# Performance work log

Measured on AMD Instinct MI355X. Metric: run time of the kernel, lower is better.

Reference implementation:

```python
import jax, jax.numpy as jnp
import numpy as np

B, N, H = 128, 1024, 128          # graphs, nodes per graph, hidden size
K1, K2, K3 = 512, 256, 128        # ceil(ratio^l * N), ratio = 0.5
DEG = 8                           # avg degree
E = B * N * DEG                   # total edges (fixed, masked after pooling)


def gcn_conv(x, row, col, mask, W, b, n):
    h = x @ W
    deg = jax.ops.segment_sum(mask, col, num_segments=n) + 1.0  # + self loop
    dinv = jax.lax.rsqrt(deg)
    coef = (dinv[row] * dinv[col] * mask)[:, None]
    agg = jax.ops.segment_sum(h[row] * coef, col, num_segments=n)
    return agg + h * (dinv * dinv)[:, None] + b  # self-loop term + bias


def topk_pool(x, row, col, mask, p, n_graphs, n_per, k):
    # PyG TopKPooling: y = x.p/||p||, keep per-graph top-k, x' = x[perm]*tanh(y[perm])
    score = (x @ p) / jnp.linalg.norm(p)
    vals, idx = jax.lax.top_k(score.reshape(n_graphs, n_per), k)  # [B, k]
    sel = (idx + (jnp.arange(n_graphs) * n_per)[:, None]).reshape(-1)
    xs = x[sel] * jnp.tanh(vals.reshape(-1))[:, None]
    # relabel edges; drop edges touching removed nodes via mask
    newid = jnp.full((n_graphs * n_per,), -1, jnp.int32).at[sel].set(
        jnp.arange(n_graphs * k, dtype=jnp.int32))
    nr, nc = newid[row], newid[col]
    nmask = mask * ((nr >= 0) & (nc >= 0)).astype(mask.dtype)
    return xs, jnp.maximum(nr, 0), jnp.maximum(nc, 0), nmask


def readout(x, n_graphs, k):
    # cat([gmp, gap]) with contiguous equal-size graphs
    xg = x.reshape(n_graphs, k, -1)
    return jnp.concatenate([xg.max(axis=1), xg.mean(axis=1)], axis=1)


def _forward(x, edge_row, edge_col, W1, b1, p1, W2, b2, p2, W3, b3, p3):
    mask = jnp.ones((E,), x.dtype)
    h = jax.nn.relu(gcn_conv(x, edge_row, edge_col, mask, W1, b1, B * N))
    x1, r, c, m = topk_pool(h, edge_row, edge_col, mask, p1, B, N, K1)
    out = readout(x1, B, K1)
    h = jax.nn.relu(gcn_conv(x1, r, c, m, W2, b2, B * K1))
    x2, r, c, m = topk_pool(h, r, c, m, p2, B, K1, K2)
    out = out + readout(x2, B, K2)
    h = jax.nn.relu(gcn_conv(x2, r, c, m, W3, b3, B * K2))
    x3, r, c, m = topk_pool(h, r, c, m, p3, B, K2, K3)
    out = out + readout(x3, B, K3)
    return out  # [B, 2*H]


def setup_inputs() -> dict:
    key = jax.random.key(0)
    ks = jax.random.split(key, 12)
    x = jax.random.normal(ks[0], (B * N, H), jnp.float32)
    off = (jnp.arange(B, dtype=jnp.int32) * N)[:, None]
    edge_row = (jax.random.randint(ks[1], (B, N * DEG), 0, N, jnp.int32) + off).reshape(-1)
    edge_col = (jax.random.randint(ks[2], (B, N * DEG), 0, N, jnp.int32) + off).reshape(-1)
    s = 1.0 / np.sqrt(H)
    params = {}
    for i, tag in enumerate(["1", "2", "3"]):
        params["W" + tag] = jax.random.normal(ks[3 + 3 * i], (H, H), jnp.float32) * s
        params["b" + tag] = jnp.zeros((H,), jnp.float32)
        params["p" + tag] = jax.random.normal(ks[4 + 3 * i], (H,), jnp.float32)
    return {"x": x, "edge_row": edge_row, "edge_col": edge_col, **params}


def reference(x, edge_row, edge_col, W1, b1, p1, W2, b2, p2, W3, b3, p3):
    return _forward(x, edge_row, edge_col, W1, b1, p1, W2, b2, p2, W3, b3, p3)
```

## Files before the change

kernel.cpp:

```cpp
#include <hip/hip_runtime.h>
#include <math.h>

#define BG   128
#define NPER 1024
#define HDIM 128
#define NEDGE (BG * NPER * 8)
#define NMAX (BG * NPER)
#define EPG  (NEDGE / BG)
#define CAP  48
#define PRE  16
#define CROWS 64

typedef __attribute__((ext_vector_type(8))) short s16x8;
typedef __attribute__((ext_vector_type(4))) float f32x4;

static __device__ __forceinline__ ushort f2bf(float f) {
  uint u = __float_as_uint(f);
  return (ushort)((u + 0x7fffu + ((u >> 16) & 1u)) >> 16);
}
static __device__ __forceinline__ float bf2f(ushort h) {
  return __uint_as_float(((uint)h) << 16);
}


__global__ __launch_bounds__(256) void countfill_kernel(
    const int* __restrict__ cr, const int* __restrict__ cc,
    int* __restrict__ cnt, int* __restrict__ meta8,
    int* __restrict__ srcext, int mask) {
  int e = blockIdx.x * 256 + threadIdx.x;
  int c = cc[e];
  int rl = cr[e] & mask;
  int pos = atomicAdd(&cnt[c], 1);
  if (pos < PRE) {
    meta8[(size_t)c * PRE + pos] = rl;
  } else if (pos < CAP) {
    srcext[(size_t)c * CAP + pos] = rl;
  }
}

extern __shared__ float ldsbuf[];


__global__ __launch_bounds__(1024) void agg_lds_kernel(
    const float* __restrict__ x, float* __restrict__ z,
    const int* __restrict__ meta8, const int* __restrict__ srcext,
    const int* __restrict__ deg, int npg) {
  float* sX = ldsbuf;
  float* sDinv = sX + npg * 32;
  int g = blockIdx.x >> 2;
  int chunk = blockIdx.x & 3;
  int t = threadIdx.x;
  int base = g * npg;

  const float4* x4 = (const float4*)x;
  float4* sX4 = (float4*)sX;
  for (int i = t; i < npg * 8; i += 1024) {
    int r = i >> 3, l8 = i & 7;
    float dv = rsqrtf((float)deg[base + r] + 1.0f);
    float4 v = x4[(size_t)(base + r) * 32 + chunk * 8 + l8];
    v.x *= dv; v.y *= dv; v.z *= dv; v.w *= dv;
    sX4[i] = v;
  }
  for (int i = t; i < npg; i += 1024)
    sDinv[i] = rsqrtf((float)deg[base + i] + 1.0f);
  __syncthreads();

  int dl = t >> 3, l = t & 7;
  int base8 = (t & 63) & 56;
  const int2* m2 = (const int2*)meta8;
  for (int dst = dl; dst < npg; dst += 128) {
    int node = base + dst;
    int2 mq = m2[(size_t)node * 8 + l];
    int d = deg[node];
    if (d > CAP) d = CAP;
    float dc = sDinv[dst];
    float4 a0 = sX4[dst * 8 + l];
    float4 a1 = make_float4(0.f, 0.f, 0.f, 0.f);
    int dp = d < PRE ? d : PRE;
    int e = 0;
    for (; e + 1 < dp; e += 2) {
      int sl = base8 + (e >> 1);
      int si0 = __shfl(mq.x, sl);
      int si1 = __shfl(mq.y, sl);
      float4 v0 = sX4[si0 * 8 + l];
      float4 v1 = sX4[si1 * 8 + l];
      a0.x += v0.x; a0.y += v0.y; a0.z += v0.z; a0.w += v0.w;
      a1.x += v1.x; a1.y += v1.y; a1.z += v1.z; a1.w += v1.w;
    }
    if (e < dp) {
      int sl = base8 + (e >> 1);
      int si0 = __shfl(mq.x, sl);
      float4 v0 = sX4[si0 * 8 + l];
      a0.x += v0.x; a0.y += v0.y; a0.z += v0.z; a0.w += v0.w;
    }
    for (int e2 = PRE; e2 < d; ++e2) {
      int rl = srcext[(size_t)node * CAP + e2];
      float4 v0 = sX4[rl * 8 + l];
      a0.x += v0.x; a0.y += v0.y; a0.z += v0.z; a0.w += v0.w;
    }
    float4 o = make_float4((a0.x + a1.x) * dc, (a0.y + a1.y) * dc,
                           (a0.z + a1.z) * dc, (a0.w + a1.w) * dc);
    ((float4*)z)[(size_t)node * 32 + chunk * 8 + l] = o;
  }
}


__global__ __launch_bounds__(256) void wsplit_kernel(
    const float* __restrict__ W0, const float* __restrict__ W1,
    const float* __restrict__ W2, ushort* __restrict__ wpk) {
  int id = blockIdx.x * 256 + threadIdx.x;
  int L = id >> 14;
  int r = id & 16383;
  int i = r & 7;
  int lane = (r >> 3) & 63;
  int nt = (r >> 9) & 7;
  int kt = (r >> 12) & 3;
  int k = kt * 32 + (lane >> 4) * 8 + i;
  int n = nt * 16 + (lane & 15);
  const float* W = (L == 0) ? W0 : (L == 1) ? W1 : W2;
  float v = W[k * HDIM + n];
  ushort h = f2bf(v);
  float r1 = v - bf2f(h);
  ushort m = f2bf(r1);
  ushort lo = f2bf(r1 - bf2f(m));
  size_t base = (size_t)L * 3 * 16384 + (size_t)r;
  wpk[base] = h;
  wpk[base + 16384] = m;
  wpk[base + 32768] = lo;
}


__global__ __launch_bounds__(256) void conv_mfma_kernel(
    float* __restrict__ zh, const ushort* __restrict__ wpk,
    const float* __restrict__ bias, const float* __restrict__ p,
    float* __restrict__ score) {
  int t = threadIdx.x;
  int wv = t >> 6, l = t & 63;
  int lr = l & 15, lq = l >> 4;
  int arow = blockIdx.x * CROWS + wv * 16 + lr;
  const float* zrow = zh + (size_t)arow * HDIM + lq * 8;

  s16x8 ah[4], am[4], al[4];
  #pragma unroll
  for (int kt = 0; kt < 4; ++kt) {
    float4 v0 = ((const float4*)(zrow + kt * 32))[0];
    float4 v1 = ((const float4*)(zrow + kt * 32))[1];
    float f[8] = {v0.x, v0.y, v0.z, v0.w, v1.x, v1.y, v1.z, v1.w};
    #pragma unroll
    for (int i = 0; i < 8; ++i) {
      ushort h = f2bf(f[i]);
      float r1 = f[i] - bf2f(h);
      ushort m = f2bf(r1);
      ushort lo = f2bf(r1 - bf2f(m));
      ah[kt][i] = (short)h; am[kt][i] = (short)m; al[kt][i] = (short)lo;
    }
  }

  f32x4 acc[8];
  #pragma unroll
  for (int nt = 0; nt < 8; ++nt) acc[nt] = (f32x4)(0.f);

  const s16x8* wh = (const s16x8*)wpk;
  const s16x8* wm = wh + 2048;
  const s16x8* wl = wm + 2048;

  #pragma unroll
  for (int kt = 0; kt < 4; ++kt) {
    #pragma unroll
    for (int nt = 0; nt < 8; ++nt) {
      int fi = (kt * 8 + nt) * 64 + l;
      s16x8 bh = wh[fi];
      s16x8 bm = wm[fi];
      s16x8 bl = wl[fi];
      acc[nt] = __builtin_amdgcn_mfma_f32_16x16x32_bf16(ah[kt], bh, acc[nt], 0, 0, 0);
      acc[nt] = __builtin_amdgcn_mfma_f32_16x16x32_bf16(ah[kt], bm, acc[nt], 0, 0, 0);
      acc[nt] = __builtin_amdgcn_mfma_f32_16x16x32_bf16(am[kt], bh, acc[nt], 0, 0, 0);
      acc[nt] = __builtin_amdgcn_mfma_f32_16x16x32_bf16(ah[kt], bl, acc[nt], 0, 0, 0);
      acc[nt] = __builtin_amdgcn_mfma_f32_16x16x32_bf16(al[kt], bh, acc[nt], 0, 0, 0);
      acc[nt] = __builtin_amdgcn_mfma_f32_16x16x32_bf16(am[kt], bm, acc[nt], 0, 0, 0);
    }
  }

  int orow = blockIdx.x * CROWS + wv * 16 + lq * 4;
  float part[4] = {0.f, 0.f, 0.f, 0.f};
  #pragma unroll
  for (int nt = 0; nt < 8; ++nt) {
    float bv = bias[nt * 16 + lr];
    float pv = p[nt * 16 + lr];
    #pragma unroll
    for (int j = 0; j < 4; ++j) {
      float hv = fmaxf(acc[nt][j] + bv, 0.f);
      part[j] += hv * pv;
      zh[(size_t)(orow + j) * HDIM + nt * 16 + lr] = hv;
    }
  }
  #pragma unroll
  for (int j = 0; j < 4; ++j) {
    #pragma unroll
    for (int s = 1; s < 16; s <<= 1) part[j] += __shfl_xor(part[j], s);
    if (lr == 0) score[orow + j] = part[j];
  }
}


__global__ __launch_bounds__(1024) void topk_mega_kernel(
    const float* __restrict__ score, const float* __restrict__ p,
    const float* __restrict__ h, float* __restrict__ xo,
    const int* __restrict__ in_r, const int* __restrict__ in_c,
    int* __restrict__ out_r, int* __restrict__ out_c,
    int* __restrict__ meta8, int* __restrict__ srcext,
    int* __restrict__ cnt, float* __restrict__ acc,
    float* __restrict__ outf, int P, int K, int L) {
  __shared__ float sv[1024];
  __shared__ int si[1024];
  __shared__ int snew[1024];
  __shared__ int scnt[512];
  __shared__ float s_pn;
  __shared__ float4 smx[32][32], ssm[32][32];
  int g = blockIdx.x;
  int t = threadIdx.x;

  if (L < 2 && t < 512) scnt[t] = 0;
  snew[t] = -1;
  if (t < 128) { float v = p[t]; sv[t] = v * v; }
  __syncthreads();
  for (int off = 64; off; off >>= 1) {
    if (t < off) sv[t] += sv[t + off];
    __syncthreads();
  }
  if (t == 0) s_pn = sqrtf(sv[0]);
  __syncthreads();
  float pn = s_pn;

  sv[t] = score[(size_t)g * P + t];
  si[t] = t;
  for (int size = 2; size <= P; size <<= 1) {
    for (int stride = size >> 1; stride; stride >>= 1) {
      __syncthreads();
      int j = t ^ stride;
      if (j > t) {
        float a = sv[t], b = sv[j];
        int ia = si[t], ib = si[j];
        bool tFirst = (a > b) || (a == b && ia < ib);
        bool up = ((t & size) == 0);
        if (up ? !tFirst : tFirst) {
          sv[t] = b; sv[j] = a;
          si[t] = ib; si[j] = ia;
        }
      }
    }
  }
  __syncthreads();
  if (t < K) {
    snew[si[t]] = t;
    sv[t] = tanhf(sv[t] / pn);
  }
  __syncthreads();

  int lane = t & 31, grp = t >> 5;
  const float4* h4 = (const float4*)h;
  float4* xo4 = (float4*)xo;
  size_t hbase = (size_t)g * P * 32;
  float4 mx = make_float4(-INFINITY, -INFINITY, -INFINITY, -INFINITY);
  float4 sm = make_float4(0.f, 0.f, 0.f, 0.f);
  #pragma unroll
  for (int i = 0; i < 16; ++i) {
    int j = grp * 16 + i;
    float th = sv[j];
    float4 v = h4[hbase + (size_t)si[j] * 32 + lane];
    v.x *= th; v.y *= th; v.z *= th; v.w *= th;
    xo4[((size_t)g * K + j) * 32 + lane] = v;
    mx.x = fmaxf(mx.x, v.x); mx.y = fmaxf(mx.y, v.y);
    mx.z = fmaxf(mx.z, v.z); mx.w = fmaxf(mx.w, v.w);
    sm.x += v.x; sm.y += v.y; sm.z += v.z; sm.w += v.w;
  }
  smx[grp][lane] = mx;
  ssm[grp][lane] = sm;
  __syncthreads();
  int ngrp = P >> 5;
  if (grp == 0) {
    for (int s2 = 1; s2 < ngrp; ++s2) {
      float4 m2 = smx[s2][lane], s3 = ssm[s2][lane];
      mx.x = fmaxf(mx.x, m2.x); mx.y = fmaxf(mx.y, m2.y);
      mx.z = fmaxf(mx.z, m2.z); mx.w = fmaxf(mx.w, m2.w);
      sm.x += s3.x; sm.y += s3.y; sm.z += s3.z; sm.w += s3.w;
    }
    int c0 = lane * 4;
    if (L < 2) {
      float* amax = acc + (size_t)L * BG * 256 + (size_t)g * 256;
      float* asum = amax + 128;
      amax[c0 + 0] = mx.x; amax[c0 + 1] = mx.y;
      amax[c0 + 2] = mx.z; amax[c0 + 3] = mx.w;
      asum[c0 + 0] = sm.x; asum[c0 + 1] = sm.y;
      asum[c0 + 2] = sm.z; asum[c0 + 3] = sm.w;
    } else {
      sv[c0 + 0] = mx.x; sv[c0 + 1] = mx.y;
      sv[c0 + 2] = mx.z; sv[c0 + 3] = mx.w;
      sv[128 + c0 + 0] = sm.x; sv[128 + c0 + 1] = sm.y;
      sv[128 + c0 + 2] = sm.z; sv[128 + c0 + 3] = sm.w;
    }
  }

  if (L == 2) {
    __syncthreads();
    float v;
    const float* a0 = acc + (size_t)g * 256;
    const float* a1 = acc + (size_t)BG * 256 + (size_t)g * 256;
    if (t < 128) {
      v = a0[t] + a1[t] + sv[t];
    } else {
      v = a0[t] * (1.f / 512.f) + a1[t] * (1.f / 256.f) + sv[t] * (1.f / 128.f);
    }
    outf[g * 256 + t] = v;
    return;
  }

  int ept = EPG / P;
  int ebase = g * EPG;
  for (int i = 0; i < ept; ++i) {
    int e = ebase + i * P + t;
    int r = in_r[e];
    int nr = -1, nc = -1;
    if (r >= 0) {
      nr = snew[r & (P - 1)];
      nc = snew[in_c[e] & (P - 1)];
    }
    bool ok = (nr >= 0) && (nc >= 0);
    out_r[e] = ok ? g * K + nr : -1;
    out_c[e] = ok ? g * K + nc : -1;
    if (ok) {
      int pos = atomicAdd(&scnt[nc], 1);
      size_t gnode = (size_t)g * K + nc;
      if (pos < PRE) {
        meta8[gnode * PRE + pos] = nr;
      } else if (pos < CAP) {
        srcext[gnode * CAP + pos] = nr;
      }
    }
  }
  __syncthreads();
  if (t < K) cnt[g * K + t] = scnt[t];
}


extern "C" void kernel_launch(void* const* d_in, const int* in_sizes, int n_in,
                              void* d_out, int out_size, void* d_ws, size_t ws_size,
                              hipStream_t stream) {
  const float* x0 = (const float*)d_in[0];
  const int* erow = (const int*)d_in[1];
  const int* ecol = (const int*)d_in[2];
  const float* Wm[3] = {(const float*)d_in[3], (const float*)d_in[6], (const float*)d_in[9]};
  const float* bm[3] = {(const float*)d_in[4], (const float*)d_in[7], (const float*)d_in[10]};
  const float* pm[3] = {(const float*)d_in[5], (const float*)d_in[8], (const float*)d_in[11]};

  char* w = (char*)d_ws;
  size_t off = 0;
  auto alloc = [&](size_t bytes) -> void* {
    void* ptr = w + off;
    off = (off + bytes + 255) & ~(size_t)255;
    return ptr;
  };
  int* cur_row = (int*)alloc((size_t)NEDGE * 4);
  int* cur_col = (int*)alloc((size_t)NEDGE * 4);
  int* meta8   = (int*)alloc((size_t)NMAX * PRE * 4);
  int* srcext  = (int*)alloc((size_t)NMAX * CAP * 4);
  int* cnt     = (int*)alloc((size_t)NMAX * 4);
  float* score = (float*)alloc((size_t)NMAX * 4);
  float* acc   = (float*)alloc((size_t)2 * BG * 256 * 4);
  float* zh    = (float*)alloc((size_t)NMAX * HDIM * 4);
  float* x1    = (float*)alloc((size_t)BG * 512 * HDIM * 4);
  float* x2    = (float*)alloc((size_t)BG * 256 * HDIM * 4);
  float* x3    = (float*)alloc((size_t)BG * 128 * HDIM * 4);
  ushort* wpk  = (ushort*)alloc((size_t)3 * 3 * 16384 * 2);

  hipFuncSetAttribute((const void*)agg_lds_kernel,
                      hipFuncAttributeMaxDynamicSharedMemorySize, 152 * 1024);

  hipMemsetAsync(cnt, 0, (size_t)NMAX * 4, stream);
  countfill_kernel<<<NEDGE / 256, 256, 0, stream>>>(erow, ecol, cnt, meta8,
                                                    srcext, NPER - 1);
  wsplit_kernel<<<(3 * 16384) / 256, 256, 0, stream>>>(Wm[0], Wm[1], Wm[2], wpk);

  const float* xin = x0;
  float* xout[3] = {x1, x2, x3};
  int Ps[3] = {1024, 512, 256};

  for (int L = 0; L < 3; ++L) {
    int P = Ps[L];
    int K = P >> 1;
    int n = BG * P;
    const int* in_r = (L == 0) ? erow : cur_row;
    const int* in_c = (L == 0) ? ecol : cur_col;
    size_t ldsBytes = (size_t)(P * 33) * 4;

    agg_lds_kernel<<<BG * 4, 1024, ldsBytes, stream>>>(
        xin, zh, meta8, srcext, cnt, P);
    conv_mfma_kernel<<<n / CROWS, 256, 0, stream>>>(
        zh, wpk + (size_t)L * 3 * 16384, bm[L], pm[L], score);
    topk_mega_kernel<<<BG, P, 0, stream>>>(
        score, pm[L], zh, xout[L], in_r, in_c, cur_row, cur_col,
        meta8, srcext, cnt, acc, (float*)d_out, P, K, L);
    xin = xout[L];
  }
}
```

Before: 373.7 us.

## Split LDS aggregation into eight feature chunks per graph with 4-wide edge unroll

The LDS-staged GCN aggregation now splits each graph's 128 features into eight 16-float chunks instead of four 32-float chunks. That halves LDS use per block (about 68KB at P=1024 instead of about 135KB) and doubles the block count, so more blocks can be resident per CU. Each destination node now uses 4 lanes instead of 8. Neighbour indices are read as int4 and unrolled four at a time with four accumulators, giving more LDS loads in flight. The cost is that the graph's degree and metadata are read twice as often in total, and lanes sit idle when a node has fewer neighbours.

```diff
diff --git a/kernel.cpp b/kernel.cpp
--- a/kernel.cpp
+++ b/kernel.cpp
@@ -46,18 +46,18 @@
     const int* __restrict__ meta8, const int* __restrict__ srcext,
     const int* __restrict__ deg, int npg) {
   float* sX = ldsbuf;
-  float* sDinv = sX + npg * 32;
-  int g = blockIdx.x >> 2;
-  int chunk = blockIdx.x & 3;
+  float* sDinv = sX + npg * 16;
+  int g = blockIdx.x >> 3;
+  int chunk = blockIdx.x & 7;
   int t = threadIdx.x;
   int base = g * npg;
 
   const float4* x4 = (const float4*)x;
   float4* sX4 = (float4*)sX;
-  for (int i = t; i < npg * 8; i += 1024) {
-    int r = i >> 3, l8 = i & 7;
+  for (int i = t; i < npg * 4; i += 1024) {
+    int r = i >> 2, j = i & 3;
     float dv = rsqrtf((float)deg[base + r] + 1.0f);
-    float4 v = x4[(size_t)(base + r) * 32 + chunk * 8 + l8];
+    float4 v = x4[(size_t)(base + r) * 32 + chunk * 4 + j];
     v.x *= dv; v.y *= dv; v.z *= dv; v.w *= dv;
     sX4[i] = v;
   }
@@ -65,42 +65,63 @@
     sDinv[i] = rsqrtf((float)deg[base + i] + 1.0f);
   __syncthreads();
 
-  int dl = t >> 3, l = t & 7;
-  int base8 = (t & 63) & 56;
-  const int2* m2 = (const int2*)meta8;
-  for (int dst = dl; dst < npg; dst += 128) {
+  int dl = t >> 2, l = t & 3;
+  int base4 = (t & 63) & 60;
+  const int4* m4 = (const int4*)meta8;
+  for (int dst = dl; dst < npg; dst += 256) {
     int node = base + dst;
-    int2 mq = m2[(size_t)node * 8 + l];
+    int4 mq = m4[(size_t)node * 4 + l];
     int d = deg[node];
     if (d > CAP) d = CAP;
     float dc = sDinv[dst];
-    float4 a0 = sX4[dst * 8 + l];
+    float4 a0 = sX4[dst * 4 + l];
     float4 a1 = make_float4(0.f, 0.f, 0.f, 0.f);
+    float4 a2 = make_float4(0.f, 0.f, 0.f, 0.f);
+    float4 a3 = make_float4(0.f, 0.f, 0.f, 0.f);
     int dp = d < PRE ? d : PRE;
-    int e = 0;
-    for (; e + 1 < dp; e += 2) {
-      int sl = base8 + (e >> 1);
-      int si0 = __shfl(mq.x, sl);
-      int si1 = __shfl(mq.y, sl);
-      float4 v0 = sX4[si0 * 8 + l];
-      float4 v1 = sX4[si1 * 8 + l];
+    int full = dp & ~3;
+    for (int e4 = 0; e4 < full; e4 += 4) {
+      int sl = base4 + (e4 >> 2);
+      int s0 = __shfl(mq.x, sl);
+      int s1 = __shfl(mq.y, sl);
+      int s2 = __shfl(mq.z, sl);
+      int s3 = __shfl(mq.w, sl);
+      float4 v0 = sX4[s0 * 4 + l];
+      float4 v1 = sX4[s1 * 4 + l];
+      float4 v2 = sX4[s2 * 4 + l];
+      float4 v3 = sX4[s3 * 4 + l];
       a0.x += v0.x; a0.y += v0.y; a0.z += v0.z; a0.w += v0.w;
       a1.x += v1.x; a1.y += v1.y; a1.z += v1.z; a1.w += v1.w;
-    }
-    if (e < dp) {
-      int sl = base8 + (e >> 1);
-      int si0 = __shfl(mq.x, sl);
-      float4 v0 = sX4[si0 * 8 + l];
+      a2.x += v2.x; a2.y += v2.y; a2.z += v2.z; a2.w += v2.w;
+      a3.x += v3.x; a3.y += v3.y; a3.z += v3.z; a3.w += v3.w;
+    }
+    int rem = dp - full;
+    if (rem) {
+      int sl = base4 + (full >> 2);
+      int s0 = __shfl(mq.x, sl);
+      int s1 = __shfl(mq.y, sl);
+      int s2 = __shfl(mq.z, sl);
+      float4 v0 = sX4[s0 * 4 + l];
       a0.x += v0.x; a0.y += v0.y; a0.z += v0.z; a0.w += v0.w;
+      if (rem > 1) {
+        float4 v1 = sX4[s1 * 4 + l];
+        a1.x += v1.x; a1.y += v1.y; a1.z += v1.z; a1.w += v1.w;
+      }
+      if (rem > 2) {
+        float4 v2 = sX4[s2 * 4 + l];
+        a2.x += v2.x; a2.y += v2.y; a2.z += v2.z; a2.w += v2.w;
+      }
     }
     for (int e2 = PRE; e2 < d; ++e2) {
       int rl = srcext[(size_t)node * CAP + e2];
-      float4 v0 = sX4[rl * 8 + l];
+      float4 v0 = sX4[rl * 4 + l];
       a0.x += v0.x; a0.y += v0.y; a0.z += v0.z; a0.w += v0.w;
     }
-    float4 o = make_float4((a0.x + a1.x) * dc, (a0.y + a1.y) * dc,
-                           (a0.z + a1.z) * dc, (a0.w + a1.w) * dc);
-    ((float4*)z)[(size_t)node * 32 + chunk * 8 + l] = o;
+    float4 o = make_float4((a0.x + a1.x + a2.x + a3.x) * dc,
+                           (a0.y + a1.y + a2.y + a3.y) * dc,
+                           (a0.z + a1.z + a2.z + a3.z) * dc,
+                           (a0.w + a1.w + a2.w + a3.w) * dc);
+    ((float4*)z)[(size_t)node * 32 + chunk * 4 + l] = o;
   }
 }
 
@@ -374,7 +395,7 @@
   ushort* wpk  = (ushort*)alloc((size_t)3 * 3 * 16384 * 2);
 
   hipFuncSetAttribute((const void*)agg_lds_kernel,
-                      hipFuncAttributeMaxDynamicSharedMemorySize, 152 * 1024);
+                      hipFuncAttributeMaxDynamicSharedMemorySize, 72 * 1024);
 
   hipMemsetAsync(cnt, 0, (size_t)NMAX * 4, stream);
   countfill_kernel<<<NEDGE / 256, 256, 0, stream>>>(erow, ecol, cnt, meta8,
@@ -391,9 +412,9 @@
     int n = BG * P;
     const int* in_r = (L == 0) ? erow : cur_row;
     const int* in_c = (L == 0) ? ecol : cur_col;
-    size_t ldsBytes = (size_t)(P * 33) * 4;
-
-    agg_lds_kernel<<<BG * 4, 1024, ldsBytes, stream>>>(
+    size_t ldsBytes = (size_t)(P * 17) * 4;
+
+    agg_lds_kernel<<<BG * 8, 1024, ldsBytes, stream>>>(
         xin, zh, meta8, srcext, cnt, P);
     conv_mfma_kernel<<<n / CROWS, 256, 0, stream>>>(
         zh, wpk + (size_t)L * 3 * 16384, bm[L], pm[L], score);
```

New measurement: 393.3 us. 5.2% more time.

## Remap agg blocks by XCD and unroll two-node branchless neighbor gather

Applied to the files above, without the earlier changes.

Each XCD now handles a contiguous set of graphs through a remapped block index, which is meant to improve L2 locality. The aggregation loop processes two destination nodes per thread group. Each thread loads all 16 prefetched neighbor indices with int4 loads instead of shuffles, and accumulates with mask-multiplied FMAs over a fully unrolled PRE loop. This adds ILP and removes shuffle and loop-branch overhead, at the cost of always doing 16 LDS reads per node, more registers, and an assumption that npg is a multiple of 256 and a power of two.

```diff
diff --git a/kernel.cpp b/kernel.cpp
--- a/kernel.cpp
+++ b/kernel.cpp
@@ -47,10 +47,13 @@
     const int* __restrict__ deg, int npg) {
   float* sX = ldsbuf;
   float* sDinv = sX + npg * 32;
-  int g = blockIdx.x >> 2;
-  int chunk = blockIdx.x & 3;
+  int b = blockIdx.x;
+  int xcd = b & 7, li = b >> 3;
+  int g = xcd * 16 + (li >> 2);
+  int chunk = li & 3;
   int t = threadIdx.x;
   int base = g * npg;
+  int nmask = npg - 1;
 
   const float4* x4 = (const float4*)x;
   float4* sX4 = (float4*)sX;
@@ -66,41 +69,78 @@
   __syncthreads();
 
   int dl = t >> 3, l = t & 7;
-  int base8 = (t & 63) & 56;
-  const int2* m2 = (const int2*)meta8;
-  for (int dst = dl; dst < npg; dst += 128) {
-    int node = base + dst;
-    int2 mq = m2[(size_t)node * 8 + l];
-    int d = deg[node];
-    if (d > CAP) d = CAP;
-    float dc = sDinv[dst];
-    float4 a0 = sX4[dst * 8 + l];
-    float4 a1 = make_float4(0.f, 0.f, 0.f, 0.f);
-    int dp = d < PRE ? d : PRE;
-    int e = 0;
-    for (; e + 1 < dp; e += 2) {
-      int sl = base8 + (e >> 1);
-      int si0 = __shfl(mq.x, sl);
-      int si1 = __shfl(mq.y, sl);
-      float4 v0 = sX4[si0 * 8 + l];
-      float4 v1 = sX4[si1 * 8 + l];
-      a0.x += v0.x; a0.y += v0.y; a0.z += v0.z; a0.w += v0.w;
-      a1.x += v1.x; a1.y += v1.y; a1.z += v1.z; a1.w += v1.w;
-    }
-    if (e < dp) {
-      int sl = base8 + (e >> 1);
-      int si0 = __shfl(mq.x, sl);
-      float4 v0 = sX4[si0 * 8 + l];
-      a0.x += v0.x; a0.y += v0.y; a0.z += v0.z; a0.w += v0.w;
-    }
-    for (int e2 = PRE; e2 < d; ++e2) {
-      int rl = srcext[(size_t)node * CAP + e2];
-      float4 v0 = sX4[rl * 8 + l];
-      a0.x += v0.x; a0.y += v0.y; a0.z += v0.z; a0.w += v0.w;
-    }
-    float4 o = make_float4((a0.x + a1.x) * dc, (a0.y + a1.y) * dc,
-                           (a0.z + a1.z) * dc, (a0.w + a1.w) * dc);
-    ((float4*)z)[(size_t)node * 32 + chunk * 8 + l] = o;
+  const int4* m4 = (const int4*)meta8;
+  float4* z4 = (float4*)z;
+
+  for (int dst0 = dl; dst0 < npg; dst0 += 256) {
+    int dA = dst0, dB = dst0 + 128;
+    int nodeA = base + dA, nodeB = base + dB;
+    int4 ia[4], ib[4];
+    #pragma unroll
+    for (int q = 0; q < 4; ++q) {
+      ia[q] = m4[(size_t)nodeA * 4 + q];
+      ib[q] = m4[(size_t)nodeB * 4 + q];
+    }
+    int dgA = deg[nodeA], dgB = deg[nodeB];
+    int dpA = dgA > PRE ? PRE : dgA;
+    int dpB = dgB > PRE ? PRE : dgB;
+    float dcA = sDinv[dA], dcB = sDinv[dB];
+    float4 accA0 = sX4[dA * 8 + l];
+    float4 accB0 = sX4[dB * 8 + l];
+    float4 accA1 = make_float4(0.f, 0.f, 0.f, 0.f);
+    float4 accB1 = make_float4(0.f, 0.f, 0.f, 0.f);
+
+    #pragma unroll
+    for (int e = 0; e < PRE; e += 2) {
+      const int q = e >> 2;
+      int sa0, sa1, sb0, sb1;
+      if ((e & 3) == 0) {
+        sa0 = ia[q].x; sa1 = ia[q].y; sb0 = ib[q].x; sb1 = ib[q].y;
+      } else {
+        sa0 = ia[q].z; sa1 = ia[q].w; sb0 = ib[q].z; sb1 = ib[q].w;
+      }
+      sa0 &= nmask; sa1 &= nmask; sb0 &= nmask; sb1 &= nmask;
+      float4 va0 = sX4[sa0 * 8 + l];
+      float4 va1 = sX4[sa1 * 8 + l];
+      float4 vb0 = sX4[sb0 * 8 + l];
+      float4 vb1 = sX4[sb1 * 8 + l];
+      float ma0 = (e < dpA) ? 1.f : 0.f;
+      float ma1 = (e + 1 < dpA) ? 1.f : 0.f;
+      float mb0 = (e < dpB) ? 1.f : 0.f;
+      float mb1 = (e + 1 < dpB) ? 1.f : 0.f;
+      accA0.x = fmaf(ma0, va0.x, accA0.x); accA0.y = fmaf(ma0, va0.y, accA0.y);
+      accA0.z = fmaf(ma0, va0.z, accA0.z); accA0.w = fmaf(ma0, va0.w, accA0.w);
+      accA1.x = fmaf(ma1, va1.x, accA1.x); accA1.y = fmaf(ma1, va1.y, accA1.y);
+      accA1.z = fmaf(ma1, va1.z, accA1.z); accA1.w = fmaf(ma1, va1.w, accA1.w);
+      accB0.x = fmaf(mb0, vb0.x, accB0.x); accB0.y = fmaf(mb0, vb0.y, accB0.y);
+      accB0.z = fmaf(mb0, vb0.z, accB0.z); accB0.w = fmaf(mb0, vb0.w, accB0.w);
+      accB1.x = fmaf(mb1, vb1.x, accB1.x); accB1.y = fmaf(mb1, vb1.y, accB1.y);
+      accB1.z = fmaf(mb1, vb1.z, accB1.z); accB1.w = fmaf(mb1, vb1.w, accB1.w);
+    }
+
+    int dxA = dgA > CAP ? CAP : dgA;
+    if (dxA > PRE) {
+      for (int e2 = PRE; e2 < dxA; ++e2) {
+        int rl = srcext[(size_t)nodeA * CAP + e2];
+        float4 v0 = sX4[rl * 8 + l];
+        accA0.x += v0.x; accA0.y += v0.y; accA0.z += v0.z; accA0.w += v0.w;
+      }
+    }
+    int dxB = dgB > CAP ? CAP : dgB;
+    if (dxB > PRE) {
+      for (int e2 = PRE; e2 < dxB; ++e2) {
+        int rl = srcext[(size_t)nodeB * CAP + e2];
+        float4 v0 = sX4[rl * 8 + l];
+        accB0.x += v0.x; accB0.y += v0.y; accB0.z += v0.z; accB0.w += v0.w;
+      }
+    }
+
+    float4 oA = make_float4((accA0.x + accA1.x) * dcA, (accA0.y + accA1.y) * dcA,
+                            (accA0.z + accA1.z) * dcA, (accA0.w + accA1.w) * dcA);
+    float4 oB = make_float4((accB0.x + accB1.x) * dcB, (accB0.y + accB1.y) * dcB,
+                            (accB0.z + accB1.z) * dcB, (accB0.w + accB1.w) * dcB);
+    z4[(size_t)nodeA * 32 + chunk * 8 + l] = oA;
+    z4[(size_t)nodeB * 32 + chunk * 8 + l] = oB;
   }
 }
 
```

Result: slower. 408.5 us (+9.3%).

## Replace LDS-staged aggregation with direct global gather plus precomputed dinv

Applied to the files above, without the earlier changes.

The aggregation kernel no longer stages a scaled quarter-feature slice of each graph into LDS. It now gathers full 128-wide rows straight from global memory (L2-resident per graph), with a warp-half per destination node and 8 blocks per graph. A separate small kernel precomputes dinv per node, and the per-source dinv is applied during accumulation via FMA. The 16 prefix edges are fully unrolled with predicated dummy loads. This removes the LDS fill, the sync and the large-LDS occupancy limit, at the cost of scattered global/L2 traffic and extra wasted loads for low-degree nodes.

```diff
diff --git a/kernel.cpp b/kernel.cpp
--- a/kernel.cpp
+++ b/kernel.cpp
@@ -38,69 +38,80 @@
   }
 }
 
-extern __shared__ float ldsbuf[];
-
-
-__global__ __launch_bounds__(1024) void agg_lds_kernel(
+
+__global__ __launch_bounds__(256) void dinv_kernel(
+    const int* __restrict__ cnt, float* __restrict__ dinv) {
+  int i = blockIdx.x * 256 + threadIdx.x;
+  dinv[i] = rsqrtf((float)cnt[i] + 1.0f);
+}
+
+
+__global__ __launch_bounds__(512, 8) void agg_gather_kernel(
     const float* __restrict__ x, float* __restrict__ z,
     const int* __restrict__ meta8, const int* __restrict__ srcext,
-    const int* __restrict__ deg, int npg) {
-  float* sX = ldsbuf;
-  float* sDinv = sX + npg * 32;
-  int g = blockIdx.x >> 2;
-  int chunk = blockIdx.x & 3;
+    const int* __restrict__ cnt, const float* __restrict__ dinv, int npg) {
+  int b = blockIdx.x;
+  int g = b >> 3, q = b & 7;
   int t = threadIdx.x;
+  int li = t & 31, gi = t >> 5;
   int base = g * npg;
+  int nmask = npg - 1;
+  int qbase = q * (npg >> 3);
+  int sl_base = t & 32;
 
   const float4* x4 = (const float4*)x;
-  float4* sX4 = (float4*)sX;
-  for (int i = t; i < npg * 8; i += 1024) {
-    int r = i >> 3, l8 = i & 7;
-    float dv = rsqrtf((float)deg[base + r] + 1.0f);
-    float4 v = x4[(size_t)(base + r) * 32 + chunk * 8 + l8];
-    v.x *= dv; v.y *= dv; v.z *= dv; v.w *= dv;
-    sX4[i] = v;
-  }
-  for (int i = t; i < npg; i += 1024)
-    sDinv[i] = rsqrtf((float)deg[base + i] + 1.0f);
-  __syncthreads();
-
-  int dl = t >> 3, l = t & 7;
-  int base8 = (t & 63) & 56;
   const int2* m2 = (const int2*)meta8;
-  for (int dst = dl; dst < npg; dst += 128) {
+  const float* dvt = dinv + base;
+  float4* z4 = (float4*)z;
+
+  int passes = npg >> 7;
+  for (int p = 0; p < passes; ++p) {
+    int dst = qbase + p * 16 + gi;
     int node = base + dst;
-    int2 mq = m2[(size_t)node * 8 + l];
-    int d = deg[node];
-    if (d > CAP) d = CAP;
-    float dc = sDinv[dst];
-    float4 a0 = sX4[dst * 8 + l];
-    float4 a1 = make_float4(0.f, 0.f, 0.f, 0.f);
-    int dp = d < PRE ? d : PRE;
-    int e = 0;
-    for (; e + 1 < dp; e += 2) {
-      int sl = base8 + (e >> 1);
-      int si0 = __shfl(mq.x, sl);
-      int si1 = __shfl(mq.y, sl);
-      float4 v0 = sX4[si0 * 8 + l];
-      float4 v1 = sX4[si1 * 8 + l];
-      a0.x += v0.x; a0.y += v0.y; a0.z += v0.z; a0.w += v0.w;
-      a1.x += v1.x; a1.y += v1.y; a1.z += v1.z; a1.w += v1.w;
-    }
-    if (e < dp) {
-      int sl = base8 + (e >> 1);
-      int si0 = __shfl(mq.x, sl);
-      float4 v0 = sX4[si0 * 8 + l];
-      a0.x += v0.x; a0.y += v0.y; a0.z += v0.z; a0.w += v0.w;
-    }
-    for (int e2 = PRE; e2 < d; ++e2) {
-      int rl = srcext[(size_t)node * CAP + e2];
-      float4 v0 = sX4[rl * 8 + l];
-      a0.x += v0.x; a0.y += v0.y; a0.z += v0.z; a0.w += v0.w;
-    }
-    float4 o = make_float4((a0.x + a1.x) * dc, (a0.y + a1.y) * dc,
-                           (a0.z + a1.z) * dc, (a0.w + a1.w) * dc);
-    ((float4*)z)[(size_t)node * 32 + chunk * 8 + l] = o;
+    int2 mq = m2[(size_t)node * 8 + (li & 7)];
+    int dg = cnt[node];
+    float dvc = dvt[dst];
+    int d = dg > CAP ? CAP : dg;
+    int dp = d > PRE ? PRE : d;
+
+    float4 vs = x4[(size_t)node * 32 + li];
+    float4 a0, a1;
+    a0.x = vs.x * dvc; a0.y = vs.y * dvc;
+    a0.z = vs.z * dvc; a0.w = vs.w * dvc;
+    a1 = make_float4(0.f, 0.f, 0.f, 0.f);
+
+    #pragma unroll
+    for (int e = 0; e < PRE; e += 2) {
+      int sl = sl_base + (e >> 1);
+      int r0 = __shfl(mq.x, sl) & nmask;
+      int r1 = __shfl(mq.y, sl) & nmask;
+      int s0 = (e < dp) ? r0 : dst;
+      int s1 = (e + 1 < dp) ? r1 : dst;
+      float4 v0 = x4[(size_t)(base + s0) * 32 + li];
+      float4 v1 = x4[(size_t)(base + s1) * 32 + li];
+      float dv0 = dvt[s0];
+      float dv1 = dvt[s1];
+      dv0 = (e < dp) ? dv0 : 0.f;
+      dv1 = (e + 1 < dp) ? dv1 : 0.f;
+      a0.x = fmaf(dv0, v0.x, a0.x); a0.y = fmaf(dv0, v0.y, a0.y);
+      a0.z = fmaf(dv0, v0.z, a0.z); a0.w = fmaf(dv0, v0.w, a0.w);
+      a1.x = fmaf(dv1, v1.x, a1.x); a1.y = fmaf(dv1, v1.y, a1.y);
+      a1.z = fmaf(dv1, v1.z, a1.z); a1.w = fmaf(dv1, v1.w, a1.w);
+    }
+
+    if (d > PRE) {
+      for (int e2 = PRE; e2 < d; ++e2) {
+        int rl = srcext[(size_t)node * CAP + e2];
+        float dv0 = dvt[rl];
+        float4 v0 = x4[(size_t)(base + rl) * 32 + li];
+        a0.x = fmaf(dv0, v0.x, a0.x); a0.y = fmaf(dv0, v0.y, a0.y);
+        a0.z = fmaf(dv0, v0.z, a0.z); a0.w = fmaf(dv0, v0.w, a0.w);
+      }
+    }
+
+    float4 o = make_float4((a0.x + a1.x) * dvc, (a0.y + a1.y) * dvc,
+                           (a0.z + a1.z) * dvc, (a0.w + a1.w) * dvc);
+    z4[(size_t)node * 32 + li] = o;
   }
 }
 
@@ -365,6 +376,7 @@
   int* meta8   = (int*)alloc((size_t)NMAX * PRE * 4);
   int* srcext  = (int*)alloc((size_t)NMAX * CAP * 4);
   int* cnt     = (int*)alloc((size_t)NMAX * 4);
+  float* dinv  = (float*)alloc((size_t)NMAX * 4);
   float* score = (float*)alloc((size_t)NMAX * 4);
   float* acc   = (float*)alloc((size_t)2 * BG * 256 * 4);
   float* zh    = (float*)alloc((size_t)NMAX * HDIM * 4);
@@ -373,9 +385,6 @@
   float* x3    = (float*)alloc((size_t)BG * 128 * HDIM * 4);
   ushort* wpk  = (ushort*)alloc((size_t)3 * 3 * 16384 * 2);
 
-  hipFuncSetAttribute((const void*)agg_lds_kernel,
-                      hipFuncAttributeMaxDynamicSharedMemorySize, 152 * 1024);
-
   hipMemsetAsync(cnt, 0, (size_t)NMAX * 4, stream);
   countfill_kernel<<<NEDGE / 256, 256, 0, stream>>>(erow, ecol, cnt, meta8,
                                                     srcext, NPER - 1);
@@ -391,10 +400,10 @@
     int n = BG * P;
     const int* in_r = (L == 0) ? erow : cur_row;
     const int* in_c = (L == 0) ? ecol : cur_col;
-    size_t ldsBytes = (size_t)(P * 33) * 4;
-
-    agg_lds_kernel<<<BG * 4, 1024, ldsBytes, stream>>>(
-        xin, zh, meta8, srcext, cnt, P);
+
+    dinv_kernel<<<n / 256, 256, 0, stream>>>(cnt, dinv);
+    agg_gather_kernel<<<BG * 8, 512, 0, stream>>>(
+        xin, zh, meta8, srcext, cnt, dinv, P);
     conv_mfma_kernel<<<n / CROWS, 256, 0, stream>>>(
         zh, wpk + (size_t)L * 3 * 16384, bm[L], pm[L], score);
     topk_mega_kernel<<<BG, P, 0, stream>>>(
```

After: 489.2 us. 30.9% more time.
